# Kernel tuning notes

Hardware: AMD Instinct MI355X
Metric: run time of the kernel (lower is better)

Reference implementation:

```python
import jax, jax.numpy as jnp
import numpy as np

N, C, NUM_ELL, E = 1024, 128, 16, 10          # nodes, channels, sum(2l+1) for lmax=3, num_elements
OUT_IRREPS = [(0, 1), (1, 3)]                  # (l_out, 2*l_out+1) for target 128x0e + 128x1o
CORRELATION = 3
NPATHS = {3: 11, 2: 4, 1: 1}                   # generalized-CG path counts per correlation order


def setup_inputs() -> dict:
    key = jax.random.key(0)
    ks = jax.random.split(key, 40)
    node_feats = jax.random.normal(ks[0], (N, C, NUM_ELL), dtype=jnp.float32)
    elem = jax.random.randint(ks[1], (N,), 0, E)
    node_attrs = jax.nn.one_hot(elem, E, dtype=jnp.float32)           # one-hot element indicator
    out_dim = C * sum(d for _, d in OUT_IRREPS)                        # 512
    sc = jax.random.normal(ks[2], (N, out_dim), dtype=jnp.float32)
    inp = {"node_feats": node_feats, "sc": sc, "node_attrs": node_attrs}
    i = 3
    for li, (_, d) in enumerate(OUT_IRREPS):
        for nu in range(1, CORRELATION + 1):
            k = NPATHS[nu]
            # U_nu: generalized CG tensor, shape [d_out, num_ell^nu ..., n_paths]
            inp[f"U_{li}_{nu}"] = jax.random.normal(ks[i], (d,) + (NUM_ELL,) * nu + (k,), dtype=jnp.float32) * np.float32(0.1)
            i += 1
            # element-indexed path weights [num_elements, n_paths, channels]
            inp[f"W_{li}_{nu}"] = jax.random.normal(ks[i], (E, k, C), dtype=jnp.float32) * np.float32(1.0 / np.sqrt(k * C))
            i += 1
        # e3nn-style per-irrep linear mixing multiplicities [C, C]
        inp[f"lin_{li}"] = jax.random.normal(ks[i], (C, C), dtype=jnp.float32)
        i += 1
    return inp


def _sym_contraction(x, y, U, W):
    # x: [N, C, num_ell], y: [N, E]; MACE Contraction recursion (highest order first)
    nu = CORRELATION
    wb = jnp.einsum("ekc,be->bkc", W[nu], y)                 # gather per-element weights
    out = jnp.einsum("...ik,bkc,bci->bc...", U[nu], wb, x)   # [N, C, d, ell, ell] for nu=3
    for nu in range(CORRELATION - 1, 0, -1):
        wb = jnp.einsum("ekc,be->bkc", W[nu], y)
        c = jnp.einsum("...k,bkc->bc...", U[nu], wb) + out
        out = jnp.einsum("bc...i,bci->bc...", c, x)          # contract one ell axis per step
    return out                                               # [N, C, d_out]


def reference(node_feats, sc, node_attrs,
              U_0_1, U_0_2, U_0_3, W_0_1, W_0_2, W_0_3, lin_0,
              U_1_1, U_1_2, U_1_3, W_1_1, W_1_2, W_1_3, lin_1):
    Us = [{1: U_0_1, 2: U_0_2, 3: U_0_3}, {1: U_1_1, 2: U_1_2, 3: U_1_3}]
    Ws = [{1: W_0_1, 2: W_0_2, 3: W_0_3}, {1: W_1_1, 2: W_1_2, 3: W_1_3}]
    lins = [lin_0, lin_1]
    inv_sqrt_c = np.float32(1.0 / np.sqrt(C))                # e3nn Linear fan-in normalization
    blocks = []
    for li in range(len(OUT_IRREPS)):
        feats = _sym_contraction(node_feats, node_attrs, Us[li], Ws[li])   # [N, C, d]
        lin_out = jnp.einsum("bcd,cf->bfd", feats, lins[li]) * inv_sqrt_c
        blocks.append(lin_out.reshape(node_feats.shape[0], -1))           # mul_ir flatten [N, C*d]
    return jnp.concatenate(blocks, axis=-1) + sc             # residual self-connection
```

## Files before the change

### kernel.cpp

```cpp
#include <hip/hip_runtime.h>

#define N_NODES 1024
#define C_CH    128
#define N_ELEM  10
#define K3      11
#define K2      4

__global__ __launch_bounds__(512) void sym_contract_kernel(
    const float* __restrict__ node_feats,
    const float* __restrict__ node_attrs,
    const float* __restrict__ U03, const float* __restrict__ W03,
    const float* __restrict__ U02, const float* __restrict__ W02,
    const float* __restrict__ U01, const float* __restrict__ W01,
    const float* __restrict__ U13, const float* __restrict__ W13,
    const float* __restrict__ U12, const float* __restrict__ W12,
    const float* __restrict__ U11, const float* __restrict__ W11,
    float* __restrict__ feats_out)
{
  __shared__ float T3s[4 * 4096];
  __shared__ float T2s[4 * 256];
  __shared__ float T1s[4 * 16];
  __shared__ float Xl[2][16][64];
  __shared__ unsigned short nodelist[N_NODES];
  __shared__ float wrow[32];
  __shared__ int cnt;

  const int e   = blockIdx.x / C_CH;
  const int c   = blockIdx.x % C_CH;
  const int tid = threadIdx.x;

  if (tid == 0) cnt = 0;
  if (tid < 32) {
    float v;
    if (tid < 11)       v = W03[(e * K3 + tid) * C_CH + c];
    else if (tid < 15)  v = W02[(e * K2 + (tid - 11)) * C_CH + c];
    else if (tid == 15) v = W01[e * C_CH + c];
    else if (tid < 27)  v = W13[(e * K3 + (tid - 16)) * C_CH + c];
    else if (tid < 31)  v = W12[(e * K2 + (tid - 27)) * C_CH + c];
    else                v = W11[e * C_CH + c];
    wrow[tid] = v;
  }
  __syncthreads();

  for (int b = tid; b < N_NODES; b += 512)
    if (node_attrs[b * N_ELEM + e] > 0.5f) {
      int p = atomicAdd(&cnt, 1);
      nodelist[p] = (unsigned short)b;
    }

  for (int s = 0; s < 4; ++s) {
    const int wb = (s == 0) ? 0 : 16;
    float wk[K3];
    #pragma unroll
    for (int k = 0; k < K3; ++k) wk[k] = wrow[wb + k];
    const float* U3 = (s == 0) ? U03 : (U13 + (size_t)(s - 1) * 4096 * K3);
    for (int w = tid; w < 4096; w += 512) {
      const float* up = U3 + (size_t)w * K3;
      float acc = 0.f;
      #pragma unroll
      for (int k = 0; k < K3; ++k) acc = fmaf(up[k], wk[k], acc);
      T3s[s * 4096 + w] = acc;
    }
  }
  for (int w = tid; w < 1024; w += 512) {
    const int m = w >> 8;
    const int r = w & 255;
    const int wb = (m == 0) ? 11 : 27;
    const float4 u2 = (m == 0)
        ? *(const float4*)(U02 + r * K2)
        : *(const float4*)(U12 + ((m - 1) * 256 + r) * K2);
    T2s[w] = u2.x * wrow[wb] + u2.y * wrow[wb + 1]
           + u2.z * wrow[wb + 2] + u2.w * wrow[wb + 3];
  }
  if (tid < 64) {
    const int m  = tid >> 4;
    const int i1 = tid & 15;
    T1s[tid] = (m == 0) ? U01[i1] * wrow[15] : U11[(m - 1) * 16 + i1] * wrow[31];
  }
  __syncthreads();

  const int wave = tid >> 6;
  const int m    = wave & 3;
  const int grp  = wave >> 2;
  const int lane = tid & 63;
  const float* T3m = T3s + m * 4096;
  const float* T2m = T2s + m * 256;
  const float* T1m = T1s + m * 16;
  const int total = cnt;

  for (int base = grp * 64; base < total; base += 128) {
    const int idx     = base + lane;
    const bool active = idx < total;
    const int b = nodelist[active ? idx : 0];
    const float* xr = node_feats + ((size_t)b * C_CH + c) * 16;
    float xs[16];
    *(float4*)&xs[0]  = ((const float4*)xr)[0];
    *(float4*)&xs[4]  = ((const float4*)xr)[1];
    *(float4*)&xs[8]  = ((const float4*)xr)[2];
    *(float4*)&xs[12] = ((const float4*)xr)[3];
    #pragma unroll
    for (int j = 0; j < 16; ++j) Xl[grp][j][lane] = xs[j];

    float s_tot = 0.f;
    for (int i1 = 0; i1 < 16; ++i1) {
      const float* t3r = T3m + i1 * 256;
      const float* t2p = T2m + i1 * 16;
      float t2r[16];
      *(float4*)&t2r[0]  = ((const float4*)t2p)[0];
      *(float4*)&t2r[4]  = ((const float4*)t2p)[1];
      *(float4*)&t2r[8]  = ((const float4*)t2p)[2];
      *(float4*)&t2r[12] = ((const float4*)t2p)[3];
      float s1 = T1m[i1];
      #pragma unroll
      for (int i2 = 0; i2 < 16; ++i2) {
        const float4 q0 = ((const float4*)(t3r + i2 * 16))[0];
        const float4 q1 = ((const float4*)(t3r + i2 * 16))[1];
        const float4 q2 = ((const float4*)(t3r + i2 * 16))[2];
        const float4 q3 = ((const float4*)(t3r + i2 * 16))[3];
        float d = t2r[i2];
        d = fmaf(q0.x, xs[0],  d); d = fmaf(q0.y, xs[1],  d);
        d = fmaf(q0.z, xs[2],  d); d = fmaf(q0.w, xs[3],  d);
        d = fmaf(q1.x, xs[4],  d); d = fmaf(q1.y, xs[5],  d);
        d = fmaf(q1.z, xs[6],  d); d = fmaf(q1.w, xs[7],  d);
        d = fmaf(q2.x, xs[8],  d); d = fmaf(q2.y, xs[9],  d);
        d = fmaf(q2.z, xs[10], d); d = fmaf(q2.w, xs[11], d);
        d = fmaf(q3.x, xs[12], d); d = fmaf(q3.y, xs[13], d);
        d = fmaf(q3.z, xs[14], d); d = fmaf(q3.w, xs[15], d);
        s1 = fmaf(d, xs[i2], s1);
      }
      const float x1v = Xl[grp][i1][lane];
      s_tot = fmaf(s1, x1v, s_tot);
    }
    if (active)
      feats_out[(size_t)b * 512 + c * 4 + m] = s_tot;
  }
}

__global__ __launch_bounds__(256) void linear_kernel(
    const float* __restrict__ sc,
    const float* __restrict__ lin0,
    const float* __restrict__ lin1,
    float* __restrict__ io)
{
  __shared__ float f[512];
  const int b   = blockIdx.x;
  const int tid = threadIdx.x;
  const float* row = io + (size_t)b * 512;
  if (tid < 128) ((float4*)f)[tid] = ((const float4*)row)[tid];
  __syncthreads();
  const float inv_sqrt_c = 0.088388347648318447f;
  #pragma unroll
  for (int rep = 0; rep < 2; ++rep) {
    const int o = tid + rep * 256;
    float acc = 0.f;
    if (o < 128) {
      const int fo = o;
      #pragma unroll 4
      for (int ci = 0; ci < 128; ++ci) acc = fmaf(f[ci * 4], lin0[ci * 128 + fo], acc);
    } else {
      const int oo = o - 128;
      const int fo = oo / 3;
      const int dd = oo - fo * 3;
      #pragma unroll 4
      for (int ci = 0; ci < 128; ++ci) acc = fmaf(f[ci * 4 + 1 + dd], lin1[ci * 128 + fo], acc);
    }
    io[(size_t)b * 512 + o] = fmaf(acc, inv_sqrt_c, sc[(size_t)b * 512 + o]);
  }
}

extern "C" void kernel_launch(void* const* d_in, const int* in_sizes, int n_in,
                              void* d_out, int out_size, void* d_ws, size_t ws_size,
                              hipStream_t stream) {
  const float* node_feats = (const float*)d_in[0];
  const float* sc         = (const float*)d_in[1];
  const float* node_attrs = (const float*)d_in[2];
  const float* U01  = (const float*)d_in[3];
  const float* W01  = (const float*)d_in[4];
  const float* U02  = (const float*)d_in[5];
  const float* W02  = (const float*)d_in[6];
  const float* U03  = (const float*)d_in[7];
  const float* W03  = (const float*)d_in[8];
  const float* lin0 = (const float*)d_in[9];
  const float* U11  = (const float*)d_in[10];
  const float* W11  = (const float*)d_in[11];
  const float* U12  = (const float*)d_in[12];
  const float* W12  = (const float*)d_in[13];
  const float* U13  = (const float*)d_in[14];
  const float* W13  = (const float*)d_in[15];
  const float* lin1 = (const float*)d_in[16];
  float* out = (float*)d_out;

  sym_contract_kernel<<<N_ELEM * C_CH, 512, 0, stream>>>(
      node_feats, node_attrs,
      U03, W03, U02, W02, U01, W01,
      U13, W13, U12, W12, U11, W11, out);
  linear_kernel<<<N_NODES, 256, 0, stream>>>(sc, lin0, lin1, out);
}
```

Before: 141.5 us.

## Symmetrize contraction tensors to exploit permutation symmetry of the cubic form

Because the contraction sums T3[i1,i2,i3]·x_i1·x_i2·x_i3, the kernel folds the 4096-entry order-3 tensor into its symmetric upper-triangular form (a>=b>=c, padded to float4 groups) and the order-2 tensor into 136 symmetric entries. The per-node inner loop then visits roughly a sixth of the multiply-adds and needs far less shared memory, and the shared Xl staging buffer is removed. In exchange the per-block setup adds a symmetrization pass with extra barriers and scalar index arithmetic, and the fully unrolled triangular loop may raise register pressure.

```diff
diff --git a/kernel.cpp b/kernel.cpp
--- a/kernel.cpp
+++ b/kernel.cpp
@@ -5,6 +5,7 @@
 #define N_ELEM  10
 #define K3      11
 #define K2      4
+#define W3PM    1040
 
 __global__ __launch_bounds__(512) void sym_contract_kernel(
     const float* __restrict__ node_feats,
@@ -17,10 +18,10 @@
     const float* __restrict__ U11, const float* __restrict__ W11,
     float* __restrict__ feats_out)
 {
-  __shared__ float T3s[4 * 4096];
-  __shared__ float T2s[4 * 256];
+  __shared__ float W3c[4 * W3PM];
+  __shared__ float Dtmp[4096];
+  __shared__ float T2c[4 * 136];
   __shared__ float T1s[4 * 16];
-  __shared__ float Xl[2][16][64];
   __shared__ unsigned short nodelist[N_NODES];
   __shared__ float wrow[32];
   __shared__ int cnt;
@@ -42,13 +43,46 @@
   }
   __syncthreads();
 
-  for (int b = tid; b < N_NODES; b += 512)
-    if (node_attrs[b * N_ELEM + e] > 0.5f) {
-      int p = atomicAdd(&cnt, 1);
-      nodelist[p] = (unsigned short)b;
-    }
+  for (int nd = tid; nd < N_NODES; nd += 512)
+    if (node_attrs[nd * N_ELEM + e] > 0.5f)
+      nodelist[atomicAdd(&cnt, 1)] = (unsigned short)nd;
+
+  for (int w = tid; w < 1024; w += 512) {
+    const int mm = w >> 8, r = w & 255;
+    const int wb = (mm == 0) ? 11 : 27;
+    const float4 u2 = (mm == 0)
+        ? *(const float4*)(U02 + r * K2)
+        : *(const float4*)(U12 + ((mm - 1) * 256 + r) * K2);
+    Dtmp[w] = u2.x * wrow[wb] + u2.y * wrow[wb + 1]
+            + u2.z * wrow[wb + 2] + u2.w * wrow[wb + 3];
+  }
+  if (tid < 64) {
+    const int mm = tid >> 4, i1 = tid & 15;
+    T1s[tid] = (mm == 0) ? U01[i1] * wrow[15] : U11[(mm - 1) * 16 + i1] * wrow[31];
+  }
+  __syncthreads();
+
+  for (int t = tid; t < 544; t += 512) {
+    const int s = t / 136;
+    int p = t - s * 136;
+    int a = 0, b = p;
+    while (b > a) { b -= (a + 1); ++a; }
+    const float* D2 = Dtmp + s * 256;
+    T2c[t] = (a == b) ? D2[a * 16 + a] : D2[a * 16 + b] + D2[b * 16 + a];
+  }
+
+  int pa = 0, pb = 0, poff = 0, prq = 0;
+  if (tid < 136) {
+    pb = tid;
+    while (pb > pa) { pb -= (pa + 1); ++pa; }
+    for (int aa = 0; aa < pa; ++aa)
+      for (int bb = 0; bb <= aa; ++bb) poff += ((bb >> 2) + 1) << 2;
+    for (int bb = 0; bb < pb; ++bb) poff += ((bb >> 2) + 1) << 2;
+    prq = ((pb >> 2) + 1) << 2;
+  }
 
   for (int s = 0; s < 4; ++s) {
+    __syncthreads();
     const int wb = (s == 0) ? 0 : 16;
     float wk[K3];
     #pragma unroll
@@ -59,23 +93,31 @@
       float acc = 0.f;
       #pragma unroll
       for (int k = 0; k < K3; ++k) acc = fmaf(up[k], wk[k], acc);
-      T3s[s * 4096 + w] = acc;
-    }
-  }
-  for (int w = tid; w < 1024; w += 512) {
-    const int m = w >> 8;
-    const int r = w & 255;
-    const int wb = (m == 0) ? 11 : 27;
-    const float4 u2 = (m == 0)
-        ? *(const float4*)(U02 + r * K2)
-        : *(const float4*)(U12 + ((m - 1) * 256 + r) * K2);
-    T2s[w] = u2.x * wrow[wb] + u2.y * wrow[wb + 1]
-           + u2.z * wrow[wb + 2] + u2.w * wrow[wb + 3];
-  }
-  if (tid < 64) {
-    const int m  = tid >> 4;
-    const int i1 = tid & 15;
-    T1s[tid] = (m == 0) ? U01[i1] * wrow[15] : U11[(m - 1) * 16 + i1] * wrow[31];
+      Dtmp[w] = acc;
+    }
+    __syncthreads();
+    if (tid < 136) {
+      const int a = pa, b = pb;
+      float* dst = W3c + s * W3PM + poff;
+      for (int cc = 0; cc < prq; ++cc) {
+        float v = 0.f;
+        if (cc <= b) {
+          if (a == b && b == cc)
+            v = Dtmp[a * 256 + a * 16 + a];
+          else if (a == b)
+            v = Dtmp[a * 256 + a * 16 + cc] + Dtmp[a * 256 + cc * 16 + a]
+              + Dtmp[cc * 256 + a * 16 + a];
+          else if (b == cc)
+            v = Dtmp[a * 256 + b * 16 + b] + Dtmp[b * 256 + a * 16 + b]
+              + Dtmp[b * 256 + b * 16 + a];
+          else
+            v = Dtmp[a * 256 + b * 16 + cc] + Dtmp[a * 256 + cc * 16 + b]
+              + Dtmp[b * 256 + a * 16 + cc] + Dtmp[b * 256 + cc * 16 + a]
+              + Dtmp[cc * 256 + a * 16 + b] + Dtmp[cc * 256 + b * 16 + a];
+        }
+        dst[cc] = v;
+      }
+    }
   }
   __syncthreads();
 
@@ -83,56 +125,46 @@
   const int m    = wave & 3;
   const int grp  = wave >> 2;
   const int lane = tid & 63;
-  const float* T3m = T3s + m * 4096;
-  const float* T2m = T2s + m * 256;
+  const float* W3m = W3c + m * W3PM;
+  const float* T2m = T2c + m * 136;
   const float* T1m = T1s + m * 16;
   const int total = cnt;
 
   for (int base = grp * 64; base < total; base += 128) {
     const int idx     = base + lane;
     const bool active = idx < total;
-    const int b = nodelist[active ? idx : 0];
-    const float* xr = node_feats + ((size_t)b * C_CH + c) * 16;
+    const int nd = nodelist[active ? idx : 0];
+    const float* xr = node_feats + ((size_t)nd * C_CH + c) * 16;
     float xs[16];
     *(float4*)&xs[0]  = ((const float4*)xr)[0];
     *(float4*)&xs[4]  = ((const float4*)xr)[1];
     *(float4*)&xs[8]  = ((const float4*)xr)[2];
     *(float4*)&xs[12] = ((const float4*)xr)[3];
+
+    float acc = 0.f;
+    int woff = 0, tp = 0;
     #pragma unroll
-    for (int j = 0; j < 16; ++j) Xl[grp][j][lane] = xs[j];
-
-    float s_tot = 0.f;
-    for (int i1 = 0; i1 < 16; ++i1) {
-      const float* t3r = T3m + i1 * 256;
-      const float* t2p = T2m + i1 * 16;
-      float t2r[16];
-      *(float4*)&t2r[0]  = ((const float4*)t2p)[0];
-      *(float4*)&t2r[4]  = ((const float4*)t2p)[1];
-      *(float4*)&t2r[8]  = ((const float4*)t2p)[2];
-      *(float4*)&t2r[12] = ((const float4*)t2p)[3];
-      float s1 = T1m[i1];
+    for (int a = 0; a < 16; ++a) {
+      float in1 = T1m[a];
       #pragma unroll
-      for (int i2 = 0; i2 < 16; ++i2) {
-        const float4 q0 = ((const float4*)(t3r + i2 * 16))[0];
-        const float4 q1 = ((const float4*)(t3r + i2 * 16))[1];
-        const float4 q2 = ((const float4*)(t3r + i2 * 16))[2];
-        const float4 q3 = ((const float4*)(t3r + i2 * 16))[3];
-        float d = t2r[i2];
-        d = fmaf(q0.x, xs[0],  d); d = fmaf(q0.y, xs[1],  d);
-        d = fmaf(q0.z, xs[2],  d); d = fmaf(q0.w, xs[3],  d);
-        d = fmaf(q1.x, xs[4],  d); d = fmaf(q1.y, xs[5],  d);
-        d = fmaf(q1.z, xs[6],  d); d = fmaf(q1.w, xs[7],  d);
-        d = fmaf(q2.x, xs[8],  d); d = fmaf(q2.y, xs[9],  d);
-        d = fmaf(q2.z, xs[10], d); d = fmaf(q2.w, xs[11], d);
-        d = fmaf(q3.x, xs[12], d); d = fmaf(q3.y, xs[13], d);
-        d = fmaf(q3.z, xs[14], d); d = fmaf(q3.w, xs[15], d);
-        s1 = fmaf(d, xs[i2], s1);
+      for (int b = 0; b <= a; ++b) {
+        float in2 = T2m[tp];
+        #pragma unroll
+        for (int q = 0; q <= (b >> 2); ++q) {
+          const float4 w4 = *(const float4*)&W3m[woff + 4 * q];
+          in2 = fmaf(w4.x, xs[4 * q + 0], in2);
+          in2 = fmaf(w4.y, xs[4 * q + 1], in2);
+          in2 = fmaf(w4.z, xs[4 * q + 2], in2);
+          in2 = fmaf(w4.w, xs[4 * q + 3], in2);
+        }
+        in1 = fmaf(in2, xs[b], in1);
+        woff += ((b >> 2) + 1) << 2;
+        ++tp;
       }
-      const float x1v = Xl[grp][i1][lane];
-      s_tot = fmaf(s1, x1v, s_tot);
+      acc = fmaf(in1, xs[a], acc);
     }
     if (active)
-      feats_out[(size_t)b * 512 + c * 4 + m] = s_tot;
+      feats_out[(size_t)nd * 512 + c * 4 + m] = acc;
   }
 }
 
```

New measurement: 217.6 us. +53.8%, slower.
